# Kernel tuning notes

Measured on AMD Instinct MI355X. Metric: run time of the kernel, lower is better.

## Reference

```python
import jax
import jax.numpy as jnp
import numpy as np

# Module configuration (matches init_kwargs)
N, C, H, W = 8, 256, 64, 64
CO, KH, KW = 256, 3, 3
SH, SW = 1, 1
PH, PW = 1, 1
DH, DW = 1, 1
G, DG = 1, 1
K = KH * KW
HO = (H + 2 * PH - (DH * (KH - 1) + 1)) // SH + 1
WO = (W + 2 * PW - (DW * (KW - 1) + 1)) // SW + 1


def setup_inputs() -> dict:
    key = jax.random.key(0)
    k1, k2, k3, k4 = jax.random.split(key, 4)
    x = jax.random.normal(k1, (N, C, H, W), dtype=jnp.float32)
    offset = jax.random.normal(k2, (N, DG * 2 * K, HO, WO), dtype=jnp.float32)
    mask = jax.random.uniform(k3, (N, DG * K, HO, WO), dtype=jnp.float32)
    stdv = 1.0 / np.sqrt(C * KH * KW)
    weight = jax.random.uniform(k4, (CO, C // G, KH, KW), dtype=jnp.float32,
                                minval=-stdv, maxval=stdv)
    return {"x": x, "offset": offset, "mask": mask, "weight": weight}


def _deform_sample(x, offset, mask):
    """Modulated deformable bilinear sampling (DCNv2 im2col).

    Returns columns [N, C, K, HO, WO].
    """
    Cg = C // DG
    # offset layout: [N, DG, K, 2(y,x), HO, WO]
    off = offset.reshape(N, DG, K, 2, HO, WO)
    off_y, off_x = off[:, :, :, 0], off[:, :, :, 1]

    # Base sampling grid per kernel tap: [K, HO, WO] broadcastable
    kgy = (jnp.repeat(jnp.arange(KH), KW) * DH).astype(jnp.float32)  # [K]
    kgx = (jnp.tile(jnp.arange(KW), KH) * DW).astype(jnp.float32)    # [K]
    oy = (jnp.arange(HO) * SH - PH).astype(jnp.float32)              # [HO]
    ox = (jnp.arange(WO) * SW - PW).astype(jnp.float32)              # [WO]
    py = kgy[:, None, None] + oy[None, :, None] + off_y  # [N,DG,K,HO,WO]
    px = kgx[:, None, None] + ox[None, None, :] + off_x  # [N,DG,K,HO,WO]

    y0 = jnp.floor(py)
    x0 = jnp.floor(px)
    ly = py - y0
    lx = px - x0
    y0i = y0.astype(jnp.int32)
    x0i = x0.astype(jnp.int32)
    y1i = y0i + 1
    x1i = x0i + 1

    xf = x.reshape(N, DG, Cg, H * W)

    def gather_one(xf_nd, idx_nd):
        # xf_nd: [Cg, H*W], idx_nd: [K*HO*WO] -> [Cg, K*HO*WO]
        return xf_nd[:, idx_nd]

    gather = jax.vmap(jax.vmap(gather_one))  # over N, DG

    def corner(yi, xi, wgt):
        valid = (yi >= 0) & (yi < H) & (xi >= 0) & (xi < W)
        yc = jnp.clip(yi, 0, H - 1)
        xc = jnp.clip(xi, 0, W - 1)
        idx = (yc * W + xc).reshape(N, DG, K * HO * WO)
        g = gather(xf, idx).reshape(N, DG, Cg, K, HO, WO)
        w = (wgt * valid.astype(x.dtype))[:, :, None]  # [N,DG,1,K,HO,WO]
        return g * w

    cols = corner(y0i, x0i, (1.0 - ly) * (1.0 - lx))
    cols = cols + corner(y0i, x1i, (1.0 - ly) * lx)
    cols = cols + corner(y1i, x0i, ly * (1.0 - lx))
    cols = cols + corner(y1i, x1i, ly * lx)

    # modulation
    m = mask.reshape(N, DG, 1, K, HO, WO)
    cols = cols * m
    return cols.reshape(N, C, K, HO, WO)


def reference(x, offset, mask, weight):
    cols = _deform_sample(x, offset, mask)              # [N,C,K,HO,WO]
    colsg = cols.reshape(N, G, C // G, K, HO, WO)
    wg = weight.reshape(G, CO // G, C // G, K)
    out = jnp.einsum('ngckhw,gock->ngohw', colsg, wg)
    return out.reshape(N, CO, HO, WO)
```

## Files before the change

### kernel.cpp

```cpp
#include <hip/hip_runtime.h>
#include <hip/hip_bf16.h>
#include <hip/hip_fp16.h>
#include <stdint.h>

#define N_   8
#define C_   256
#define H_   64
#define W_   64
#define CO_  256
#define K_   9
#define HO_  64
#define WO_  64
#define CK_  (C_ * K_)
#define P_   (HO_ * WO_)

#define BN   128
#define BK   64
#define NT   36
#define NTHR 512

typedef __attribute__((ext_vector_type(8))) _Float16 f16x8;
typedef __attribute__((ext_vector_type(4))) float f32x4;

__device__ __forceinline__ unsigned short f2bf(float f) {
    uint32_t u = __builtin_bit_cast(uint32_t, f);
    uint32_t r = (u + 0x7FFFu + ((u >> 16) & 1u)) >> 16;
    return (unsigned short)r;
}
__device__ __forceinline__ float bf2f(unsigned short u) {
    return __builtin_bit_cast(float, (uint32_t)u << 16);
}
__device__ __forceinline__ unsigned short f2h(float f) {
    return __builtin_bit_cast(unsigned short, (_Float16)f);
}


__global__ __launch_bounds__(256)
void transpose_x(const float* __restrict__ x, unsigned short* __restrict__ xT) {
    __shared__ float t[64][65];
    const int n  = blockIdx.z;
    const int c0 = blockIdx.y * 64;
    const int h0 = blockIdx.x * 64;
    const int tx = threadIdx.x & 63;
    const int ty = threadIdx.x >> 6;
    const float* xp = x + ((size_t)n * C_ + c0) * P_ + h0;
    #pragma unroll
    for (int i = 0; i < 16; ++i) {
        int c = ty * 16 + i;
        t[c][tx] = xp[(size_t)c * P_ + tx];
    }
    __syncthreads();
    unsigned short* op = xT + ((size_t)n * P_ + h0) * C_ + c0;
    #pragma unroll
    for (int i = 0; i < 16; ++i) {
        int hw = ty * 16 + i;
        op[(size_t)hw * C_ + tx] = f2h(t[tx][hw]);
    }
}

__global__ __launch_bounds__(256)
void reorder_w(const float* __restrict__ w, unsigned short* __restrict__ Wt) {
    const int co = blockIdx.x;
    const int c  = threadIdx.x;
    const float* src = w + (size_t)co * CK_ + (size_t)c * K_;
    float v[9];
    #pragma unroll
    for (int k = 0; k < 9; ++k) v[k] = src[k];
    #pragma unroll
    for (int k = 0; k < 9; ++k)
        Wt[(size_t)co * CK_ + k * C_ + c] = f2h(v[k]);
}

__device__ __forceinline__ void barrier_lgkm_only() {
    __builtin_amdgcn_sched_barrier(0);
    asm volatile("s_waitcnt lgkmcnt(0)" ::: "memory");
    __builtin_amdgcn_s_barrier();
    __builtin_amdgcn_sched_barrier(0);
}

#define COMB(dst, A, B, Cc, D) do {                                   \
    __half2 _v = __hmul2(W0, __builtin_bit_cast(__half2, (A)));       \
    _v = __hfma2(W1, __builtin_bit_cast(__half2, (B)), _v);           \
    _v = __hfma2(W2, __builtin_bit_cast(__half2, (Cc)), _v);          \
    _v = __hfma2(W3, __builtin_bit_cast(__half2, (D)), _v);           \
    (dst) = __builtin_bit_cast(unsigned, _v); } while (0)

__global__ __launch_bounds__(NTHR, 2)
void dcn_main(const unsigned short* __restrict__ xT,
              const unsigned short* __restrict__ Wt,
              const float* __restrict__ offset,
              const float* __restrict__ mask,
              float* __restrict__ out) {
    __shared__ uint2 sIdx[BN * K_];
    __shared__ uint4 sWd [BN * K_];
    __shared__ unsigned short sWs[CO_ * BK];
    __shared__ unsigned short sBs[BN * BK];

    const int tid = threadIdx.x;
    const int bid = blockIdx.x;
    const int n   = bid & 7;
    const int p0  = (bid >> 3) * BN;

    for (int e = tid; e < BN * K_; e += NTHR) {
        int pl = e / K_;
        int k  = e - pl * K_;
        int p  = p0 + pl;
        int ho = p >> 6, wo = p & 63;
        float offy = offset[(size_t)((n * 2 * K_ + 2 * k)     * P_) + p];
        float offx = offset[(size_t)((n * 2 * K_ + 2 * k + 1) * P_) + p];
        float m    = mask  [(size_t)((n * K_ + k) * P_) + p];
        float py = (float)(k / 3 + ho - 1) + offy;
        float px = (float)(k % 3 + wo - 1) + offx;
        float y0f = floorf(py), x0f = floorf(px);
        float ly = py - y0f,   lx = px - x0f;
        int y0 = (int)y0f, x0 = (int)x0f;
        int y1 = y0 + 1,   x1 = x0 + 1;
        bool vy0 = (y0 >= 0) & (y0 < H_);
        bool vy1 = (y1 >= 0) & (y1 < H_);
        bool vx0 = (x0 >= 0) & (x0 < W_);
        bool vx1 = (x1 >= 0) & (x1 < W_);
        float w00 = (1.f - ly) * (1.f - lx) * m * ((vy0 & vx0) ? 1.f : 0.f);
        float w01 = (1.f - ly) * lx         * m * ((vy0 & vx1) ? 1.f : 0.f);
        float w10 = ly * (1.f - lx)         * m * ((vy1 & vx0) ? 1.f : 0.f);
        float w11 = ly * lx                 * m * ((vy1 & vx1) ? 1.f : 0.f);
        unsigned int cy0 = (unsigned)min(max(y0, 0), H_ - 1);
        unsigned int cy1 = (unsigned)min(max(y1, 0), H_ - 1);
        unsigned int cx0 = (unsigned)min(max(x0, 0), W_ - 1);
        unsigned int cx1 = (unsigned)min(max(x1, 0), W_ - 1);
        sIdx[e] = make_uint2((cy0 * W_ + cx0) | ((cy0 * W_ + cx1) << 16),
                             (cy1 * W_ + cx0) | ((cy1 * W_ + cx1) << 16));
        sWd[e] = make_uint4((unsigned)f2h(w00) * 0x10001u,
                            (unsigned)f2h(w01) * 0x10001u,
                            (unsigned)f2h(w10) * 0x10001u,
                            (unsigned)f2h(w11) * 0x10001u);
    }
    __syncthreads();

    const unsigned short* xTn = xT + (size_t)n * P_ * C_;

    const int spl  = tid >> 2;
    const int cs16 = (tid & 3) * 16;
    const int bsw  = spl & 7;
    char* bdst0 = (char*)sBs + spl * 128 + ((((tid & 3) * 2)     ^ bsw) << 4);
    char* bdst1 = (char*)sBs + spl * 128 + ((((tid & 3) * 2 + 1) ^ bsw) << 4);
    const int wco  = tid >> 1;
    const int wchq = (tid & 1) * 4;
    const int wswz = wco & 7;
    char* wrow = (char*)sWs + wco * 128;
    const unsigned short* wsrcbase = Wt + (size_t)wco * CK_ + (tid & 1) * 32;

    const int lane = tid & 63;
    const int wid  = tid >> 6;
    const int wm   = (wid & 3) * 64;
    const int wp   = (wid >> 2) * 64;
    const int l15  = lane & 15;
    const int l4   = lane >> 4;
    const int slA  = l4 ^ (l15 & 7);

    f32x4 acc[4][4] = {};

    uint4 qa0, qa1, qb0, qb1, qc0, qc1, qd0, qd1;
    uint4 wq0, wq1, wq2, wq3;

    {
        const unsigned short* ws = wsrcbase;
        wq0 = *(const uint4*)(ws);
        wq1 = *(const uint4*)(ws + 8);
        wq2 = *(const uint4*)(ws + 16);
        wq3 = *(const uint4*)(ws + 24);
        uint2 id = sIdx[spl * K_];
        const unsigned short* base = xTn + cs16;
        const unsigned short* ba = base + ((size_t)(id.x & 0xFFFFu) << 8);
        const unsigned short* bb = base + ((size_t)(id.x >> 16)     << 8);
        const unsigned short* bc = base + ((size_t)(id.y & 0xFFFFu) << 8);
        const unsigned short* bd = base + ((size_t)(id.y >> 16)     << 8);
        qa0 = *(const uint4*)(ba); qa1 = *(const uint4*)(ba + 8);
        qb0 = *(const uint4*)(bb); qb1 = *(const uint4*)(bb + 8);
        qc0 = *(const uint4*)(bc); qc1 = *(const uint4*)(bc + 8);
        qd0 = *(const uint4*)(bd); qd1 = *(const uint4*)(bd + 8);
    }

    for (int t = 0; t < NT; ++t) {
        const int k = t >> 2;

        barrier_lgkm_only();

        asm volatile("s_waitcnt vmcnt(0)" ::: "memory");

        {
            *(uint4*)(wrow + (((wchq + 0) ^ wswz) << 4)) = wq0;
            *(uint4*)(wrow + (((wchq + 1) ^ wswz) << 4)) = wq1;
            *(uint4*)(wrow + (((wchq + 2) ^ wswz) << 4)) = wq2;
            *(uint4*)(wrow + (((wchq + 3) ^ wswz) << 4)) = wq3;

            uint4 wv = sWd[spl * K_ + k];
            __half2 W0 = __builtin_bit_cast(__half2, wv.x);
            __half2 W1 = __builtin_bit_cast(__half2, wv.y);
            __half2 W2 = __builtin_bit_cast(__half2, wv.z);
            __half2 W3 = __builtin_bit_cast(__half2, wv.w);
            uint4 r0, r1;
            COMB(r0.x, qa0.x, qb0.x, qc0.x, qd0.x);
            COMB(r0.y, qa0.y, qb0.y, qc0.y, qd0.y);
            COMB(r0.z, qa0.z, qb0.z, qc0.z, qd0.z);
            COMB(r0.w, qa0.w, qb0.w, qc0.w, qd0.w);
            COMB(r1.x, qa1.x, qb1.x, qc1.x, qd1.x);
            COMB(r1.y, qa1.y, qb1.y, qc1.y, qd1.y);
            COMB(r1.z, qa1.z, qb1.z, qc1.z, qd1.z);
            COMB(r1.w, qa1.w, qb1.w, qc1.w, qd1.w);
            *(uint4*)bdst0 = r0;
            *(uint4*)bdst1 = r1;
        }

        if (t + 1 < NT) {
            const int kn  = (t + 1) >> 2;
            const int c0n = ((t + 1) & 3) * 64;
            const unsigned short* ws = wsrcbase + kn * C_ + c0n;
            wq0 = *(const uint4*)(ws);
            wq1 = *(const uint4*)(ws + 8);
            wq2 = *(const uint4*)(ws + 16);
            wq3 = *(const uint4*)(ws + 24);
            uint2 id = sIdx[spl * K_ + kn];
            const unsigned short* base = xTn + c0n + cs16;
            const unsigned short* ba = base + ((size_t)(id.x & 0xFFFFu) << 8);
            const unsigned short* bb = base + ((size_t)(id.x >> 16)     << 8);
            const unsigned short* bc = base + ((size_t)(id.y & 0xFFFFu) << 8);
            const unsigned short* bd = base + ((size_t)(id.y >> 16)     << 8);
            qa0 = *(const uint4*)(ba); qa1 = *(const uint4*)(ba + 8);
            qb0 = *(const uint4*)(bb); qb1 = *(const uint4*)(bb + 8);
            qc0 = *(const uint4*)(bc); qc1 = *(const uint4*)(bc + 8);
            qd0 = *(const uint4*)(bd); qd1 = *(const uint4*)(bd + 8);
        }

        barrier_lgkm_only();

        #pragma unroll
        for (int ks = 0; ks < 2; ++ks) {
            const int sl = slA ^ (ks << 2);
            f16x8 b0 = *(const f16x8*)((const char*)sBs + (wp      + l15) * 128 + (sl << 4));
            f16x8 b1 = *(const f16x8*)((const char*)sBs + (wp + 16 + l15) * 128 + (sl << 4));
            f16x8 b2 = *(const f16x8*)((const char*)sBs + (wp + 32 + l15) * 128 + (sl << 4));
            f16x8 b3 = *(const f16x8*)((const char*)sBs + (wp + 48 + l15) * 128 + (sl << 4));
            #pragma unroll
            for (int m = 0; m < 4; ++m) {
                f16x8 a = *(const f16x8*)((const char*)sWs + (wm + m * 16 + l15) * 128 + (sl << 4));
                acc[m][0] = __builtin_amdgcn_mfma_f32_16x16x32_f16(a, b0, acc[m][0], 0, 0, 0);
                acc[m][1] = __builtin_amdgcn_mfma_f32_16x16x32_f16(a, b1, acc[m][1], 0, 0, 0);
                acc[m][2] = __builtin_amdgcn_mfma_f32_16x16x32_f16(a, b2, acc[m][2], 0, 0, 0);
                acc[m][3] = __builtin_amdgcn_mfma_f32_16x16x32_f16(a, b3, acc[m][3], 0, 0, 0);
            }
        }
    }

    float* outn = out + (size_t)n * CO_ * P_;
    #pragma unroll
    for (int m = 0; m < 4; ++m) {
        int co = wm + m * 16 + l4 * 4;
        #pragma unroll
        for (int nn = 0; nn < 4; ++nn) {
            int p = p0 + wp + nn * 16 + l15;
            #pragma unroll
            for (int r = 0; r < 4; ++r) {
                outn[(size_t)(co + r) * P_ + p] = acc[m][nn][r];
            }
        }
    }
}

template <int TAG>
__global__ __launch_bounds__(512, 2)
void dcn_fb(const float* __restrict__ x,
            const float* __restrict__ offset,
            const float* __restrict__ mask,
            const float* __restrict__ weight,
            float* __restrict__ out) {
    typedef __attribute__((ext_vector_type(8))) short bf16x8;
    __shared__ uint2  sIdx[128 * K_];
    __shared__ float4 sW  [128 * K_];
    __shared__ unsigned short sWs[CO_ * 32];
    __shared__ unsigned short sBs[128 * 32];

    const int tid = threadIdx.x;
    const int n  = blockIdx.y;
    const int p0 = blockIdx.x * 128;

    for (int e = tid; e < 128 * K_; e += 512) {
        int pl = e / K_;
        int k  = e - pl * K_;
        int p  = p0 + pl;
        int ho = p >> 6, wo = p & 63;
        float offy = offset[(size_t)((n * 2 * K_ + 2 * k)     * P_) + p];
        float offx = offset[(size_t)((n * 2 * K_ + 2 * k + 1) * P_) + p];
        float m    = mask  [(size_t)((n * K_ + k) * P_) + p];
        float py = (float)(k / 3 + ho - 1) + offy;
        float px = (float)(k % 3 + wo - 1) + offx;
        float y0f = floorf(py), x0f = floorf(px);
        float ly = py - y0f,   lx = px - x0f;
        int y0 = (int)y0f, x0 = (int)x0f;
        int y1 = y0 + 1,   x1 = x0 + 1;
        bool vy0 = (y0 >= 0) & (y0 < H_);
        bool vy1 = (y1 >= 0) & (y1 < H_);
        bool vx0 = (x0 >= 0) & (x0 < W_);
        bool vx1 = (x1 >= 0) & (x1 < W_);
        float w00 = (1.f - ly) * (1.f - lx) * m * ((vy0 & vx0) ? 1.f : 0.f);
        float w01 = (1.f - ly) * lx         * m * ((vy0 & vx1) ? 1.f : 0.f);
        float w10 = ly * (1.f - lx)         * m * ((vy1 & vx0) ? 1.f : 0.f);
        float w11 = ly * lx                 * m * ((vy1 & vx1) ? 1.f : 0.f);
        unsigned int cy0 = (unsigned)min(max(y0, 0), H_ - 1);
        unsigned int cy1 = (unsigned)min(max(y1, 0), H_ - 1);
        unsigned int cx0 = (unsigned)min(max(x0, 0), W_ - 1);
        unsigned int cx1 = (unsigned)min(max(x1, 0), W_ - 1);
        sIdx[e] = make_uint2((cy0 * W_ + cx0) | ((cy0 * W_ + cx1) << 16),
                             (cy1 * W_ + cx0) | ((cy1 * W_ + cx1) << 16));
        sW[e]   = make_float4(w00, w01, w10, w11);
    }

    const float* xn = x + (size_t)n * C_ * P_;
    const int pl   = tid >> 2;
    const int pl9  = pl * K_;
    const int ckb  = (tid & 3) * 8;
    const int wco  = tid >> 1;
    const int wck  = (tid & 1) * 16;

    const int lane = tid & 63;
    const int wid  = tid >> 6;
    const int wm   = (wid & 1) * 128;
    const int wp   = (wid >> 1) * 32;
    const int l15  = lane & 15;
    const int l4   = lane >> 4;

    f32x4 acc[8][2] = {};

    for (int ck0 = 0; ck0 < CK_; ck0 += 32) {
        __syncthreads();
        {
            const float4* wsrc = (const float4*)(weight + (size_t)wco * CK_ + ck0 + wck);
            float4 wa = wsrc[0], wb = wsrc[1], wc = wsrc[2], wd = wsrc[3];
            uint4 q0, q1;
            q0.x = f2bf(wa.x) | ((unsigned)f2bf(wa.y) << 16);
            q0.y = f2bf(wa.z) | ((unsigned)f2bf(wa.w) << 16);
            q0.z = f2bf(wb.x) | ((unsigned)f2bf(wb.y) << 16);
            q0.w = f2bf(wb.z) | ((unsigned)f2bf(wb.w) << 16);
            q1.x = f2bf(wc.x) | ((unsigned)f2bf(wc.y) << 16);
            q1.y = f2bf(wc.z) | ((unsigned)f2bf(wc.w) << 16);
            q1.z = f2bf(wd.x) | ((unsigned)f2bf(wd.y) << 16);
            q1.w = f2bf(wd.z) | ((unsigned)f2bf(wd.w) << 16);
            *(uint4*)&sWs[wco * 32 + wck]     = q0;
            *(uint4*)&sWs[wco * 32 + wck + 8] = q1;
        }
        {
            int ckstart = ck0 + ckb;
            int cc = ckstart / 9;
            int kk = ckstart - cc * 9;
            unsigned int packed[4];
            unsigned short colv[8];
            #pragma unroll
            for (int j = 0; j < 8; ++j) {
                int e = pl9 + kk;
                uint2  id = sIdx[e];
                float4 wv = sW[e];
                const float* xp = xn + ((size_t)cc << 12);
                float v = wv.x * xp[id.x & 0xFFFFu]
                        + wv.y * xp[id.x >> 16]
                        + wv.z * xp[id.y & 0xFFFFu]
                        + wv.w * xp[id.y >> 16];
                colv[j] = f2bf(v);
                ++kk; if (kk == 9) { kk = 0; ++cc; }
            }
            packed[0] = colv[0] | ((unsigned)colv[1] << 16);
            packed[1] = colv[2] | ((unsigned)colv[3] << 16);
            packed[2] = colv[4] | ((unsigned)colv[5] << 16);
            packed[3] = colv[6] | ((unsigned)colv[7] << 16);
            *(uint4*)&sBs[pl * 32 + ckb] = *(uint4*)packed;
        }
        __syncthreads();
        bf16x8 bfr0 = *(const bf16x8*)&sBs[(wp + l15)      * 32 + l4 * 8];
        bf16x8 bfr1 = *(const bf16x8*)&sBs[(wp + 16 + l15) * 32 + l4 * 8];
        #pragma unroll
        for (int m = 0; m < 8; ++m) {
            bf16x8 afr = *(const bf16x8*)&sWs[(wm + m * 16 + l15) * 32 + l4 * 8];
            acc[m][0] = __builtin_amdgcn_mfma_f32_16x16x32_bf16(afr, bfr0, acc[m][0], 0, 0, 0);
            acc[m][1] = __builtin_amdgcn_mfma_f32_16x16x32_bf16(afr, bfr1, acc[m][1], 0, 0, 0);
        }
    }

    float* outn = out + (size_t)n * CO_ * P_;
    #pragma unroll
    for (int m = 0; m < 8; ++m) {
        int co = wm + m * 16 + l4 * 4;
        #pragma unroll
        for (int nn = 0; nn < 2; ++nn) {
            int p = p0 + wp + nn * 16 + l15;
            #pragma unroll
            for (int r = 0; r < 4; ++r) {
                outn[(size_t)(co + r) * P_ + p] = acc[m][nn][r];
            }
        }
    }
}

extern "C" void kernel_launch(void* const* d_in, const int* in_sizes, int n_in,
                              void* d_out, int out_size, void* d_ws, size_t ws_size,
                              hipStream_t stream) {
    const float* x      = (const float*)d_in[0];
    const float* offset = (const float*)d_in[1];
    const float* mask   = (const float*)d_in[2];
    const float* weight = (const float*)d_in[3];
    float* out = (float*)d_out;

    const size_t xT_elems = (size_t)N_ * P_ * C_;
    const size_t Wt_elems = (size_t)CO_ * CK_;
    const size_t need     = (xT_elems + Wt_elems) * sizeof(unsigned short);

    if (ws_size >= need) {
        unsigned short* xT = (unsigned short*)d_ws;
        unsigned short* Wt = xT + xT_elems;
        transpose_x<<<dim3(P_ / 64, C_ / 64, N_), dim3(256), 0, stream>>>(x, xT);
        reorder_w<<<dim3(CO_), dim3(256), 0, stream>>>(weight, Wt);
        dcn_main<<<dim3((P_ / BN) * N_), dim3(NTHR), 0, stream>>>(xT, Wt, offset, mask, out);
    } else if (ws_size >= (8u << 20)) {
        dcn_fb<1><<<dim3(P_ / 128, N_), dim3(512), 0, stream>>>(x, offset, mask, weight, out);
    } else {
        dcn_fb<0><<<dim3(P_ / 128, N_), dim3(512), 0, stream>>>(x, offset, mask, weight, out);
    }
}
```

Before: 83.87 us.

## Double-buffer LDS tiles to drop one barrier per K-step

Doubles the weight and sampled-column LDS buffers so that the next tile is blended and stored into the alternate buffer while the current tile is read for MFMA. This removes the second barrier per iteration and lets global prefetch run two steps ahead, overlapping the gather/blend with matrix math. LDS use per block roughly doubles, from about 57KB to about 106KB, which may cut occupancy below two blocks per CU. Fragment loads also move into registers ahead of the MFMAs, which raises register pressure.

```diff
diff --git a/kernel.cpp b/kernel.cpp
--- a/kernel.cpp
+++ b/kernel.cpp
@@ -93,8 +93,8 @@
               float* __restrict__ out) {
     __shared__ uint2 sIdx[BN * K_];
     __shared__ uint4 sWd [BN * K_];
-    __shared__ unsigned short sWs[CO_ * BK];
-    __shared__ unsigned short sBs[BN * BK];
+    __shared__ unsigned short sWs[2][CO_ * BK];
+    __shared__ unsigned short sBs[2][BN * BK];
 
     const int tid = threadIdx.x;
     const int bid = blockIdx.x;
@@ -141,12 +141,12 @@
     const int spl  = tid >> 2;
     const int cs16 = (tid & 3) * 16;
     const int bsw  = spl & 7;
-    char* bdst0 = (char*)sBs + spl * 128 + ((((tid & 3) * 2)     ^ bsw) << 4);
-    char* bdst1 = (char*)sBs + spl * 128 + ((((tid & 3) * 2 + 1) ^ bsw) << 4);
+    const int boff0 = spl * 128 + ((((tid & 3) * 2)     ^ bsw) << 4);
+    const int boff1 = spl * 128 + ((((tid & 3) * 2 + 1) ^ bsw) << 4);
     const int wco  = tid >> 1;
     const int wchq = (tid & 1) * 4;
     const int wswz = wco & 7;
-    char* wrow = (char*)sWs + wco * 128;
+    const int woff = wco * 128;
     const unsigned short* wsrcbase = Wt + (size_t)wco * CK_ + (tid & 1) * 32;
 
     const int lane = tid & 63;
@@ -162,94 +162,116 @@
     uint4 qa0, qa1, qb0, qb1, qc0, qc1, qd0, qd1;
     uint4 wq0, wq1, wq2, wq3;
 
-    {
-        const unsigned short* ws = wsrcbase;
-        wq0 = *(const uint4*)(ws);
-        wq1 = *(const uint4*)(ws + 8);
-        wq2 = *(const uint4*)(ws + 16);
-        wq3 = *(const uint4*)(ws + 24);
-        uint2 id = sIdx[spl * K_];
-        const unsigned short* base = xTn + cs16;
-        const unsigned short* ba = base + ((size_t)(id.x & 0xFFFFu) << 8);
-        const unsigned short* bb = base + ((size_t)(id.x >> 16)     << 8);
-        const unsigned short* bc = base + ((size_t)(id.y & 0xFFFFu) << 8);
-        const unsigned short* bd = base + ((size_t)(id.y >> 16)     << 8);
-        qa0 = *(const uint4*)(ba); qa1 = *(const uint4*)(ba + 8);
-        qb0 = *(const uint4*)(bb); qb1 = *(const uint4*)(bb + 8);
-        qc0 = *(const uint4*)(bc); qc1 = *(const uint4*)(bc + 8);
-        qd0 = *(const uint4*)(bd); qd1 = *(const uint4*)(bd + 8);
-    }
+#define PREF(TT) {                                                        \
+        const int kn  = (TT) >> 2;                                        \
+        const int c0n = ((TT) & 3) * 64;                                  \
+        const unsigned short* ws = wsrcbase + kn * C_ + c0n;              \
+        wq0 = *(const uint4*)(ws);                                        \
+        wq1 = *(const uint4*)(ws + 8);                                    \
+        wq2 = *(const uint4*)(ws + 16);                                   \
+        wq3 = *(const uint4*)(ws + 24);                                   \
+        uint2 id = sIdx[spl * K_ + kn];                                   \
+        const unsigned short* base = xTn + c0n + cs16;                    \
+        const unsigned short* ba = base + ((size_t)(id.x & 0xFFFFu) << 8);\
+        const unsigned short* bb = base + ((size_t)(id.x >> 16)     << 8);\
+        const unsigned short* bc = base + ((size_t)(id.y & 0xFFFFu) << 8);\
+        const unsigned short* bd = base + ((size_t)(id.y >> 16)     << 8);\
+        qa0 = *(const uint4*)(ba); qa1 = *(const uint4*)(ba + 8);         \
+        qb0 = *(const uint4*)(bb); qb1 = *(const uint4*)(bb + 8);         \
+        qc0 = *(const uint4*)(bc); qc1 = *(const uint4*)(bc + 8);         \
+        qd0 = *(const uint4*)(bd); qd1 = *(const uint4*)(bd + 8);         \
+    }
+
+#define STAGE(TT, WB, BB) {                                               \
+        asm volatile("s_waitcnt vmcnt(0)" ::: "memory");                  \
+        char* wrB = (char*)(WB) + woff;                                   \
+        *(uint4*)(wrB + (((wchq + 0) ^ wswz) << 4)) = wq0;                \
+        *(uint4*)(wrB + (((wchq + 1) ^ wswz) << 4)) = wq1;                \
+        *(uint4*)(wrB + (((wchq + 2) ^ wswz) << 4)) = wq2;                \
+        *(uint4*)(wrB + (((wchq + 3) ^ wswz) << 4)) = wq3;                \
+        uint4 wv = sWd[spl * K_ + ((TT) >> 2)];                           \
+        __half2 W0 = __builtin_bit_cast(__half2, wv.x);                   \
+        __half2 W1 = __builtin_bit_cast(__half2, wv.y);                   \
+        __half2 W2 = __builtin_bit_cast(__half2, wv.z);                   \
+        __half2 W3 = __builtin_bit_cast(__half2, wv.w);                   \
+        uint4 r0, r1;                                                     \
+        COMB(r0.x, qa0.x, qb0.x, qc0.x, qd0.x);                           \
+        COMB(r0.y, qa0.y, qb0.y, qc0.y, qd0.y);                           \
+        COMB(r0.z, qa0.z, qb0.z, qc0.z, qd0.z);                           \
+        COMB(r0.w, qa0.w, qb0.w, qc0.w, qd0.w);                           \
+        COMB(r1.x, qa1.x, qb1.x, qc1.x, qd1.x);                           \
+        COMB(r1.y, qa1.y, qb1.y, qc1.y, qd1.y);                           \
+        COMB(r1.z, qa1.z, qb1.z, qc1.z, qd1.z);                           \
+        COMB(r1.w, qa1.w, qb1.w, qc1.w, qd1.w);                           \
+        *(uint4*)((char*)(BB) + boff0) = r0;                              \
+        *(uint4*)((char*)(BB) + boff1) = r1;                              \
+    }
+
+    PREF(0)
+    STAGE(0, sWs[0], sBs[0])
+    PREF(1)
 
     for (int t = 0; t < NT; ++t) {
-        const int k = t >> 2;
+        const int br = t & 1;
+        const int bw = br ^ 1;
+        const char* wR = (const char*)sWs[br];
+        const char* bR = (const char*)sBs[br];
 
         barrier_lgkm_only();
 
-        asm volatile("s_waitcnt vmcnt(0)" ::: "memory");
-
+        f16x8 a0[2], a1[2], a2[2], a3[2], b0[2], b1[2], b2[2], b3[2];
         {
-            *(uint4*)(wrow + (((wchq + 0) ^ wswz) << 4)) = wq0;
-            *(uint4*)(wrow + (((wchq + 1) ^ wswz) << 4)) = wq1;
-            *(uint4*)(wrow + (((wchq + 2) ^ wswz) << 4)) = wq2;
-            *(uint4*)(wrow + (((wchq + 3) ^ wswz) << 4)) = wq3;
-
-            uint4 wv = sWd[spl * K_ + k];
-            __half2 W0 = __builtin_bit_cast(__half2, wv.x);
-            __half2 W1 = __builtin_bit_cast(__half2, wv.y);
-            __half2 W2 = __builtin_bit_cast(__half2, wv.z);
-            __half2 W3 = __builtin_bit_cast(__half2, wv.w);
-            uint4 r0, r1;
-            COMB(r0.x, qa0.x, qb0.x, qc0.x, qd0.x);
-            COMB(r0.y, qa0.y, qb0.y, qc0.y, qd0.y);
-            COMB(r0.z, qa0.z, qb0.z, qc0.z, qd0.z);
-            COMB(r0.w, qa0.w, qb0.w, qc0.w, qd0.w);
-            COMB(r1.x, qa1.x, qb1.x, qc1.x, qd1.x);
-            COMB(r1.y, qa1.y, qb1.y, qc1.y, qd1.y);
-            COMB(r1.z, qa1.z, qb1.z, qc1.z, qd1.z);
-            COMB(r1.w, qa1.w, qb1.w, qc1.w, qd1.w);
-            *(uint4*)bdst0 = r0;
-            *(uint4*)bdst1 = r1;
+            const int sl = slA;
+            b0[0] = *(const f16x8*)(bR + (wp      + l15) * 128 + (sl << 4));
+            b1[0] = *(const f16x8*)(bR + (wp + 16 + l15) * 128 + (sl << 4));
+            b2[0] = *(const f16x8*)(bR + (wp + 32 + l15) * 128 + (sl << 4));
+            b3[0] = *(const f16x8*)(bR + (wp + 48 + l15) * 128 + (sl << 4));
+            a0[0] = *(const f16x8*)(wR + (wm      + l15) * 128 + (sl << 4));
+            a1[0] = *(const f16x8*)(wR + (wm + 16 + l15) * 128 + (sl << 4));
+            a2[0] = *(const f16x8*)(wR + (wm + 32 + l15) * 128 + (sl << 4));
+            a3[0] = *(const f16x8*)(wR + (wm + 48 + l15) * 128 + (sl << 4));
         }
 
         if (t + 1 < NT) {
-            const int kn  = (t + 1) >> 2;
-            const int c0n = ((t + 1) & 3) * 64;
-            const unsigned short* ws = wsrcbase + kn * C_ + c0n;
-            wq0 = *(const uint4*)(ws);
-            wq1 = *(const uint4*)(ws + 8);
-            wq2 = *(const uint4*)(ws + 16);
-            wq3 = *(const uint4*)(ws + 24);
-            uint2 id = sIdx[spl * K_ + kn];
-            const unsigned short* base = xTn + c0n + cs16;
-            const unsigned short* ba = base + ((size_t)(id.x & 0xFFFFu) << 8);
-            const unsigned short* bb = base + ((size_t)(id.x >> 16)     << 8);
-            const unsigned short* bc = base + ((size_t)(id.y & 0xFFFFu) << 8);
-            const unsigned short* bd = base + ((size_t)(id.y >> 16)     << 8);
-            qa0 = *(const uint4*)(ba); qa1 = *(const uint4*)(ba + 8);
-            qb0 = *(const uint4*)(bb); qb1 = *(const uint4*)(bb + 8);
-            qc0 = *(const uint4*)(bc); qc1 = *(const uint4*)(bc + 8);
-            qd0 = *(const uint4*)(bd); qd1 = *(const uint4*)(bd + 8);
-        }
-
-        barrier_lgkm_only();
+            if (br) { STAGE(t + 1, sWs[0], sBs[0]) }
+            else    { STAGE(t + 1, sWs[1], sBs[1]) }
+            if (t + 2 < NT) PREF(t + 2)
+        }
+
+        {
+            const int sl = slA ^ 4;
+            b0[1] = *(const f16x8*)(bR + (wp      + l15) * 128 + (sl << 4));
+            b1[1] = *(const f16x8*)(bR + (wp + 16 + l15) * 128 + (sl << 4));
+            b2[1] = *(const f16x8*)(bR + (wp + 32 + l15) * 128 + (sl << 4));
+            b3[1] = *(const f16x8*)(bR + (wp + 48 + l15) * 128 + (sl << 4));
+            a0[1] = *(const f16x8*)(wR + (wm      + l15) * 128 + (sl << 4));
+            a1[1] = *(const f16x8*)(wR + (wm + 16 + l15) * 128 + (sl << 4));
+            a2[1] = *(const f16x8*)(wR + (wm + 32 + l15) * 128 + (sl << 4));
+            a3[1] = *(const f16x8*)(wR + (wm + 48 + l15) * 128 + (sl << 4));
+        }
 
         #pragma unroll
         for (int ks = 0; ks < 2; ++ks) {
-            const int sl = slA ^ (ks << 2);
-            f16x8 b0 = *(const f16x8*)((const char*)sBs + (wp      + l15) * 128 + (sl << 4));
-            f16x8 b1 = *(const f16x8*)((const char*)sBs + (wp + 16 + l15) * 128 + (sl << 4));
-            f16x8 b2 = *(const f16x8*)((const char*)sBs + (wp + 32 + l15) * 128 + (sl << 4));
-            f16x8 b3 = *(const f16x8*)((const char*)sBs + (wp + 48 + l15) * 128 + (sl << 4));
-            #pragma unroll
-            for (int m = 0; m < 4; ++m) {
-                f16x8 a = *(const f16x8*)((const char*)sWs + (wm + m * 16 + l15) * 128 + (sl << 4));
-                acc[m][0] = __builtin_amdgcn_mfma_f32_16x16x32_f16(a, b0, acc[m][0], 0, 0, 0);
-                acc[m][1] = __builtin_amdgcn_mfma_f32_16x16x32_f16(a, b1, acc[m][1], 0, 0, 0);
-                acc[m][2] = __builtin_amdgcn_mfma_f32_16x16x32_f16(a, b2, acc[m][2], 0, 0, 0);
-                acc[m][3] = __builtin_amdgcn_mfma_f32_16x16x32_f16(a, b3, acc[m][3], 0, 0, 0);
-            }
-        }
-    }
+            acc[0][0] = __builtin_amdgcn_mfma_f32_16x16x32_f16(a0[ks], b0[ks], acc[0][0], 0, 0, 0);
+            acc[0][1] = __builtin_amdgcn_mfma_f32_16x16x32_f16(a0[ks], b1[ks], acc[0][1], 0, 0, 0);
+            acc[0][2] = __builtin_amdgcn_mfma_f32_16x16x32_f16(a0[ks], b2[ks], acc[0][2], 0, 0, 0);
+            acc[0][3] = __builtin_amdgcn_mfma_f32_16x16x32_f16(a0[ks], b3[ks], acc[0][3], 0, 0, 0);
+            acc[1][0] = __builtin_amdgcn_mfma_f32_16x16x32_f16(a1[ks], b0[ks], acc[1][0], 0, 0, 0);
+            acc[1][1] = __builtin_amdgcn_mfma_f32_16x16x32_f16(a1[ks], b1[ks], acc[1][1], 0, 0, 0);
+            acc[1][2] = __builtin_amdgcn_mfma_f32_16x16x32_f16(a1[ks], b2[ks], acc[1][2], 0, 0, 0);
+            acc[1][3] = __builtin_amdgcn_mfma_f32_16x16x32_f16(a1[ks], b3[ks], acc[1][3], 0, 0, 0);
+            acc[2][0] = __builtin_amdgcn_mfma_f32_16x16x32_f16(a2[ks], b0[ks], acc[2][0], 0, 0, 0);
+            acc[2][1] = __builtin_amdgcn_mfma_f32_16x16x32_f16(a2[ks], b1[ks], acc[2][1], 0, 0, 0);
+            acc[2][2] = __builtin_amdgcn_mfma_f32_16x16x32_f16(a2[ks], b2[ks], acc[2][2], 0, 0, 0);
+            acc[2][3] = __builtin_amdgcn_mfma_f32_16x16x32_f16(a2[ks], b3[ks], acc[2][3], 0, 0, 0);
+            acc[3][0] = __builtin_amdgcn_mfma_f32_16x16x32_f16(a3[ks], b0[ks], acc[3][0], 0, 0, 0);
+            acc[3][1] = __builtin_amdgcn_mfma_f32_16x16x32_f16(a3[ks], b1[ks], acc[3][1], 0, 0, 0);
+            acc[3][2] = __builtin_amdgcn_mfma_f32_16x16x32_f16(a3[ks], b2[ks], acc[3][2], 0, 0, 0);
+            acc[3][3] = __builtin_amdgcn_mfma_f32_16x16x32_f16(a3[ks], b3[ks], acc[3][3], 0, 0, 0);
+        }
+    }
+#undef PREF
+#undef STAGE
 
     float* outn = out + (size_t)n * CO_ * P_;
     #pragma unroll
```

Measured after the change: 72.29 us. 1.16x faster.
